# Performance work log

Measured on AMD Instinct MI355X. Metric: run time of the kernel, lower is better.

## Reference

```python
import jax, jax.numpy as jnp
import numpy as np

B = 64           # number of graphs
MAXN = 128       # max nodes per graph (== to_dense_batch n)
D = 512          # hidden_dim
H = 16           # n_attn_heads
HS = D // H      # head_size
SCALE = HS ** -0.5
EPS = 1e-5

# deterministic ragged node counts in [64,128], max exactly 128
_COUNTS = 64 + (np.arange(B) * 37) % 65
NTOT = int(_COUNTS.sum())  # 6148


def setup_inputs() -> dict:
    key = jax.random.key(0)
    ks = jax.random.split(key, 10)
    r = D ** -0.5  # uniform init radius used by the module

    def lin(k):
        kw, kb = jax.random.split(k)
        W = jax.random.uniform(kw, (D, D), minval=-r, maxval=r, dtype=jnp.float32)
        b = jax.random.uniform(kb, (D,), minval=-r, maxval=r, dtype=jnp.float32)
        return W, b

    Wq, bq = lin(ks[0])
    Wk, bk = lin(ks[1])
    Wv, bv = lin(ks[2])
    Wp, bp = lin(ks[3])
    x = jax.random.normal(ks[4], (NTOT, D), dtype=jnp.float32)
    attn_bias = 0.1 * jax.random.normal(ks[5], (B, H, MAXN, MAXN), dtype=jnp.float32)
    batch = jnp.asarray(np.repeat(np.arange(B), _COUNTS), dtype=jnp.int32)
    return {
        "x": x, "attn_bias": attn_bias,
        "Wq": Wq, "bq": bq, "Wk": Wk, "bk": bk, "Wv": Wv, "bv": bv,
        "Wp": Wp, "bp": bp,
        "ln_w": jnp.ones((D,), jnp.float32), "ln_b": jnp.zeros((D,), jnp.float32),
        "batch": batch,
    }


def reference(x, attn_bias, Wq, bq, Wk, bk, Wv, bv, Wp, bp, ln_w, ln_b, batch):
    # eval-mode BiasedSelfAttentionLayer (all dropouts are identity)
    Bn, Hh, n, _ = attn_bias.shape
    N = x.shape[0]
    # to_dense_batch: per-node position inside its graph
    counts = jax.ops.segment_sum(jnp.ones(N, jnp.int32), batch, num_segments=Bn)
    starts = jnp.cumsum(counts) - counts
    pos = jnp.arange(N) - starts[batch]
    x_dense = jnp.zeros((Bn, n, D), x.dtype).at[batch, pos].set(x)  # [B,n,D]
    mask = jnp.zeros((Bn, n), bool).at[batch, pos].set(True)        # [B,n]

    def heads(W, b):
        return (x_dense @ W.T + b).reshape(Bn, n, Hh, HS).transpose(0, 2, 1, 3)

    q = heads(Wq, bq)  # [B,H,n,hs]
    k = heads(Wk, bk)
    v = heads(Wv, bv)

    attn = jnp.einsum("bhqd,bhkd->bhqk", q, k) * SCALE + attn_bias  # [B,H,n,n]
    mask2 = mask[:, None, :, None]  # valid queries
    mask3 = mask[:, None, None, :]  # valid keys
    attn = jnp.where(mask3, attn, -jnp.inf)   # masked_fill(~mask3, -inf)
    attn = jnp.where(mask2, attn, 0.0)        # masked_fill(~mask2, 0.0)
    attn = jax.nn.softmax(attn, axis=-1)
    attn = jnp.where(mask2, attn, 0.0)        # re-zero invalid query rows

    out = jnp.einsum("bhqk,bhkd->bhqd", attn, v)           # [B,H,n,hs]
    out = out.transpose(0, 2, 1, 3).reshape(Bn, n, D)      # [B,n,D]
    out = out @ Wp.T + bp
    out = out[batch, pos] + x                               # scatter back + residual
    # LayerNorm
    mu = out.mean(-1, keepdims=True)
    var = out.var(-1, keepdims=True)
    return (out - mu) / jnp.sqrt(var + EPS) * ln_w + ln_b
```

## Files before the change

### kernel.cpp

```cpp
#include <hip/hip_runtime.h>
#include <math.h>

#define NTOT 6148
#define NB 64
#define DM 512
#define SCALE_F 0.17677669529663687f

typedef __attribute__((ext_vector_type(8))) short bf16x8;
typedef __attribute__((ext_vector_type(4))) float f32x4;

__device__ __forceinline__ short f2bf(float f) {
  union { float f; unsigned u; } v; v.f = f;
  unsigned r = (v.u + 0x7fffu + ((v.u >> 16) & 1u)) >> 16;
  return (short)r;
}

__device__ __forceinline__ void gl_lds16(const void* g, void* l) {
  auto gp = (const __attribute__((address_space(1))) unsigned*)(unsigned long long)(uintptr_t)g;
  auto lp = (__attribute__((address_space(3))) unsigned*)(unsigned long long)(uintptr_t)l;
  __builtin_amdgcn_global_load_lds(gp, lp, 16, 0, 0);
}

__global__ __launch_bounds__(256) void k_cvt(const float* __restrict__ x,
                                             const float* __restrict__ wq,
                                             const float* __restrict__ wk,
                                             const float* __restrict__ wv,
                                             const float* __restrict__ wp,
                                             short* __restrict__ xb,
                                             short* __restrict__ wqb,
                                             short* __restrict__ wkb,
                                             short* __restrict__ wvb,
                                             short* __restrict__ wpb,
                                             const int* __restrict__ batch,
                                             int* __restrict__ starts) {
  const int bid = blockIdx.x;
  if (bid < 25) {
    const int i = bid * 256 + threadIdx.x;
    if (i < NTOT) {
      const int bb = batch[i];
      if (i == 0) starts[bb] = 0;
      else if (batch[i - 1] != bb) starts[bb] = i;
      if (i == NTOT - 1) starts[NB] = NTOT;
    }
  }
  const float* s; short* d; long off;
  if (bid < 1537) {
    s = x; d = xb;
    off = ((long)bid * 256 + threadIdx.x) * 8;
  } else {
    int wi = (bid - 1537) >> 7;
    s = (wi == 0) ? wq : (wi == 1) ? wk : (wi == 2) ? wv : wp;
    d = (wi == 0) ? wqb : (wi == 1) ? wkb : (wi == 2) ? wvb : wpb;
    off = ((long)((bid - 1537) & 127) * 256 + threadIdx.x) * 8;
  }
  float4 v0 = *(const float4*)(s + off);
  float4 v1 = *(const float4*)(s + off + 4);
  bf16x8 o;
  o[0] = f2bf(v0.x); o[1] = f2bf(v0.y); o[2] = f2bf(v0.z); o[3] = f2bf(v0.w);
  o[4] = f2bf(v1.x); o[5] = f2bf(v1.y); o[6] = f2bf(v1.z); o[7] = f2bf(v1.w);
  *(bf16x8*)(d + off) = o;
}

template <int NT, bool BF16OUT>
__global__ __launch_bounds__(256) void k_gemm_mfma(
    const short* __restrict__ Abf,
    const short* __restrict__ W0, const short* __restrict__ W1, const short* __restrict__ W2,
    const float* __restrict__ b0, const float* __restrict__ b1, const float* __restrict__ b2,
    const float* __restrict__ resid, void* __restrict__ Cv, int ldc, int M) {
  constexpr int NF = NT / 32;
  __shared__ __align__(16) short As[2][64][32];
  __shared__ __align__(16) short Bs[2][NT][32];
  const int tid = threadIdx.x;
  const int w = tid >> 6, l = tid & 63;
  const int m0 = blockIdx.y * 64;
  const int n0 = blockIdx.x * NT;
  const int sel = n0 >> 9;
  const short* Wt = (sel == 0) ? W0 : (sel == 1) ? W1 : W2;
  const float* bt = (sel == 0) ? b0 : (sel == 1) ? b1 : b2;
  const int nl0 = n0 & 511;
  const int wr = w >> 1, wc = w & 1;
  const int lr = l >> 2;
  const int lc = (l & 3) * 8;
  const int fr = l & 15, fs = (l >> 4) * 8;

  const long gaA = (long)min(m0 + w * 16 + lr, M - 1) * 512 + lc;
  const long gaB0 = (long)(nl0 + ((NT == 128) ? w * 32 : w * 16) + lr) * 512 + lc;
  const long gaB1 = (long)(nl0 + w * 32 + 16 + lr) * 512 + lc;

  f32x4 acc[2][NF];
#pragma unroll
  for (int m = 0; m < 2; m++)
#pragma unroll
    for (int n = 0; n < NF; n++) acc[m][n] = (f32x4){0.f, 0.f, 0.f, 0.f};

  auto stage = [&](int kt, int buf) {
    const int k0 = kt * 32;
    gl_lds16(Abf + gaA + k0, &As[buf][w * 16][0]);
    if (NT == 128) {
      gl_lds16(Wt + gaB0 + k0, &Bs[buf][w * 32][0]);
      gl_lds16(Wt + gaB1 + k0, &Bs[buf][w * 32 + 16][0]);
    } else {
      gl_lds16(Wt + gaB0 + k0, &Bs[buf][w * 16][0]);
    }
  };
  auto compute = [&](int buf) {
    bf16x8 af[2], bfr[NF];
#pragma unroll
    for (int m = 0; m < 2; m++) af[m] = *(const bf16x8*)&As[buf][wr * 32 + m * 16 + fr][fs];
#pragma unroll
    for (int n = 0; n < NF; n++)
      bfr[n] = *(const bf16x8*)&Bs[buf][wc * (NT / 2) + n * 16 + fr][fs];
#pragma unroll
    for (int m = 0; m < 2; m++)
#pragma unroll
      for (int n = 0; n < NF; n++)
        acc[m][n] = __builtin_amdgcn_mfma_f32_16x16x32_bf16(af[m], bfr[n], acc[m][n], 0, 0, 0);
  };

  stage(0, 0);
  __syncthreads();
  for (int step = 0; step < 16; step++) {
    if (step < 15) stage(step + 1, (step + 1) & 1);
    compute(step & 1);
    __syncthreads();
  }

  const int er = (l >> 4) * 4, ec = l & 15;
#pragma unroll
  for (int n = 0; n < NF; n++) {
    const int col = n0 + wc * (NT / 2) + n * 16 + ec;
    const float bv = bt[col & 511];
#pragma unroll
    for (int m = 0; m < 2; m++) {
      const int rowb = m0 + wr * 32 + m * 16 + er;
#pragma unroll
      for (int j = 0; j < 4; j++) {
        const int row = rowb + j;
        if (row < M) {
          float v = acc[m][n][j] + bv;
          if (resid) v += resid[(long)row * 512 + col];
          if (BF16OUT) ((short*)Cv)[(long)row * ldc + col] = f2bf(v);
          else ((float*)Cv)[(long)row * ldc + col] = v;
        }
      }
    }
  }
}

__global__ __launch_bounds__(256, 2) void k_attn(const short* __restrict__ QKVbf,
                                                 const float* __restrict__ bias,
                                                 const int* __restrict__ starts,
                                                 short* __restrict__ Obf) {
  __shared__ __align__(16) short Ps[4][16][136];
  __shared__ __align__(16) short Vtb[32][136];
  const int id = blockIdx.x;
  const int wg = (id & 7) * 256 + (id >> 3);
  const int b = wg >> 5, qc = (wg >> 4) & 1, h = wg & 15;
  const int tid = threadIdx.x, l = tid & 63, w = tid >> 6;
  const int wq0 = qc * 64 + w * 16;
  const int lg = l >> 4, lk = l & 15, fs = lg * 8;

  const int s0 = starts[b], cnt = starts[b + 1] - s0;
  const bool active = wq0 < cnt;

  const int u = l >> 2, c = (l & 3) * 8;
  const int vr0 = w * 32 + u, vr1 = vr0 + 16;
  const short* vbase = QKVbf + 1024 + h * 32 + c;
  const bf16x8 v0 = *(const bf16x8*)(vbase + (long)(s0 + min(vr0, cnt - 1)) * 1536);
  const bf16x8 v1 = *(const bf16x8*)(vbase + (long)(s0 + min(vr1, cnt - 1)) * 1536);

  bf16x8 aq, bk[8];
  float bv[8][4];
  if (active) {
    const short* qbase = QKVbf + h * 32 + fs;
    aq = *(const bf16x8*)(qbase + (long)(s0 + min(wq0 + lk, cnt - 1)) * 1536);
#pragma unroll
    for (int n = 0; n < 8; n++)
      bk[n] = *(const bf16x8*)(qbase + 512 + (long)(s0 + min(n * 16 + lk, cnt - 1)) * 1536);
    const float* bb = bias + ((long)(b * 16 + h) << 14) + (long)(wq0 + lg * 4) * 128 + lk;
#pragma unroll
    for (int n = 0; n < 8; n++)
#pragma unroll
      for (int j = 0; j < 4; j++) bv[n][j] = bb[j * 128 + n * 16];
  }

#pragma unroll
  for (int i = 0; i < 8; i++) Vtb[c + i][vr0] = v0[i];
#pragma unroll
  for (int i = 0; i < 8; i++) Vtb[c + i][vr1] = v1[i];

  float invs[4];
  if (active) {
    f32x4 S[8];
#pragma unroll
    for (int n = 0; n < 8; n++)
      S[n] = __builtin_amdgcn_mfma_f32_16x16x32_bf16(aq, bk[n],
                                                     (f32x4){0.f, 0.f, 0.f, 0.f}, 0, 0, 0);
#pragma unroll
    for (int n = 0; n < 8; n++) {
      const int k = n * 16 + lk;
      const bool kok = k < cnt;
#pragma unroll
      for (int j = 0; j < 4; j++) {
        const float sv = S[n][j] * SCALE_F + bv[n][j];
        S[n][j] = kok ? sv : -1e30f;
      }
    }
#pragma unroll
    for (int j = 0; j < 4; j++) {
      float mx = S[0][j];
#pragma unroll
      for (int n = 1; n < 8; n++) mx = fmaxf(mx, S[n][j]);
      mx = fmaxf(mx, __shfl_xor(mx, 1));
      mx = fmaxf(mx, __shfl_xor(mx, 2));
      mx = fmaxf(mx, __shfl_xor(mx, 4));
      mx = fmaxf(mx, __shfl_xor(mx, 8));
      float sum = 0.f;
#pragma unroll
      for (int n = 0; n < 8; n++) {
        const float p = __expf(S[n][j] - mx);
        S[n][j] = p;
        sum += p;
      }
      sum += __shfl_xor(sum, 1);
      sum += __shfl_xor(sum, 2);
      sum += __shfl_xor(sum, 4);
      sum += __shfl_xor(sum, 8);
      invs[j] = 1.f / sum;
      const int r = lg * 4 + j;
#pragma unroll
      for (int n = 0; n < 8; n++) Ps[w][r][n * 16 + lk] = f2bf(S[n][j]);
    }
  }

  __syncthreads();
  if (!active) return;

  f32x4 O[2];
#pragma unroll
  for (int dt = 0; dt < 2; dt++) O[dt] = (f32x4){0.f, 0.f, 0.f, 0.f};
#pragma unroll
  for (int kc = 0; kc < 4; kc++) {
    const bf16x8 pa = *(const bf16x8*)&Ps[w][lk][kc * 32 + fs];
#pragma unroll
    for (int dt = 0; dt < 2; dt++) {
      const bf16x8 vb = *(const bf16x8*)&Vtb[dt * 16 + lk][kc * 32 + fs];
      O[dt] = __builtin_amdgcn_mfma_f32_16x16x32_bf16(pa, vb, O[dt], 0, 0, 0);
    }
  }
#pragma unroll
  for (int j = 0; j < 4; j++) {
    const int q = wq0 + lg * 4 + j;
    if (q < cnt) {
      short* orow = Obf + (long)(s0 + q) * 512 + h * 32;
#pragma unroll
      for (int dt = 0; dt < 2; dt++)
        orow[dt * 16 + lk] = f2bf(O[dt][j] * invs[j]);
    }
  }
}

__global__ __launch_bounds__(256) void k_lnp(const float* __restrict__ pre,
                                             const float* __restrict__ lw,
                                             const float* __restrict__ lb,
                                             float* __restrict__ out) {
  const int row = blockIdx.x * 4 + (threadIdx.x >> 6);
  if (row >= NTOT) return;
  const int lane = threadIdx.x & 63;
  const float* pr = pre + (long)row * 512 + lane * 8;
  float4 p0 = *(const float4*)pr;
  float4 p1 = *(const float4*)(pr + 4);
  float v[8] = {p0.x, p0.y, p0.z, p0.w, p1.x, p1.y, p1.z, p1.w};
  float s = 0.f, s2 = 0.f;
#pragma unroll
  for (int j = 0; j < 8; j++) { s += v[j]; s2 += v[j] * v[j]; }
#pragma unroll
  for (int off = 32; off > 0; off >>= 1) {
    s += __shfl_xor(s, off);
    s2 += __shfl_xor(s2, off);
  }
  const float mu = s * (1.f / 512.f);
  const float var = s2 * (1.f / 512.f) - mu * mu;
  const float inv = rsqrtf(var + 1e-5f);
  float4 w0 = *(const float4*)&lw[lane * 8];
  float4 w1 = *(const float4*)&lw[lane * 8 + 4];
  float4 b0 = *(const float4*)&lb[lane * 8];
  float4 b1 = *(const float4*)&lb[lane * 8 + 4];
  float4 o0 = make_float4((v[0] - mu) * inv * w0.x + b0.x, (v[1] - mu) * inv * w0.y + b0.y,
                          (v[2] - mu) * inv * w0.z + b0.z, (v[3] - mu) * inv * w0.w + b0.w);
  float4 o1 = make_float4((v[4] - mu) * inv * w1.x + b1.x, (v[5] - mu) * inv * w1.y + b1.y,
                          (v[6] - mu) * inv * w1.z + b1.z, (v[7] - mu) * inv * w1.w + b1.w);
  float* dst = out + (long)row * 512 + lane * 8;
  *(float4*)dst = o0;
  *(float4*)(dst + 4) = o1;
}

extern "C" void kernel_launch(void* const* d_in, const int* in_sizes, int n_in,
                              void* d_out, int out_size, void* d_ws, size_t ws_size,
                              hipStream_t stream) {
  const float* x = (const float*)d_in[0];
  const float* attn_bias = (const float*)d_in[1];
  const float* Wq = (const float*)d_in[2];
  const float* bq = (const float*)d_in[3];
  const float* Wk = (const float*)d_in[4];
  const float* bk = (const float*)d_in[5];
  const float* Wv = (const float*)d_in[6];
  const float* bv = (const float*)d_in[7];
  const float* Wp = (const float*)d_in[8];
  const float* bp = (const float*)d_in[9];
  const float* ln_w = (const float*)d_in[10];
  const float* ln_b = (const float*)d_in[11];
  const int* batch = (const int*)d_in[12];
  float* out = (float*)d_out;

  char* ws = (char*)d_ws;
  int* starts = (int*)ws;
  short* Xbf = (short*)(ws + 512);
  short* Wqb = Xbf + (long)NTOT * 512;
  short* Wkb = Wqb + 512 * 512;
  short* Wvb = Wkb + 512 * 512;
  short* Wpb = Wvb + 512 * 512;
  short* QKVbf = Wpb + 512 * 512;
  short* Obf = Xbf;
  float* proj = (float*)QKVbf;

  k_cvt<<<1537 + 4 * 128, 256, 0, stream>>>(x, Wq, Wk, Wv, Wp, Xbf, Wqb, Wkb, Wvb, Wpb,
                                            batch, starts);

  dim3 gq(12, (NTOT + 63) / 64);
  k_gemm_mfma<128, true><<<gq, 256, 0, stream>>>(Xbf, Wqb, Wkb, Wvb, bq, bk, bv,
                                                 nullptr, QKVbf, 1536, NTOT);

  k_attn<<<2048, 256, 0, stream>>>(QKVbf, attn_bias, starts, Obf);

  dim3 gp(8, (NTOT + 63) / 64);
  k_gemm_mfma<64, false><<<gp, 256, 0, stream>>>(Obf, Wpb, Wpb, Wpb, bp, bp, bp,
                                                 x, proj, 512, NTOT);

  k_lnp<<<(NTOT + 3) / 4, 256, 0, stream>>>(proj, ln_w, ln_b, out);
}
```

Baseline: 75.60 us.

## Transpose score MFMA for vectorized bias loads and store bf16 projection output

The QK^T MFMA operands are swapped so each lane holds four consecutive keys for one query row. This lets the attention bias be read as float4, the softmax reductions need only two cross-lane shuffles, and probabilities can be normalized before being written to LDS as bf16x4. Separately, the output projection GEMM now writes bf16 instead of fp32, which halves the traffic into the LayerNorm kernel. That bf16 intermediate, which includes the residual, reduces precision before LayerNorm. It is also unclear whether the bf16 GEMM template path adds x as a residual the same way the fp32 path did.

```diff
diff --git a/kernel.cpp b/kernel.cpp
--- a/kernel.cpp
+++ b/kernel.cpp
@@ -7,12 +7,18 @@
 #define SCALE_F 0.17677669529663687f
 
 typedef __attribute__((ext_vector_type(8))) short bf16x8;
+typedef __attribute__((ext_vector_type(4))) short bf16x4;
 typedef __attribute__((ext_vector_type(4))) float f32x4;
 
 __device__ __forceinline__ short f2bf(float f) {
   union { float f; unsigned u; } v; v.f = f;
   unsigned r = (v.u + 0x7fffu + ((v.u >> 16) & 1u)) >> 16;
   return (short)r;
+}
+__device__ __forceinline__ float bf2f(short s) {
+  union { unsigned u; float f; } v;
+  v.u = ((unsigned)(unsigned short)s) << 16;
+  return v.f;
 }
 
 __device__ __forceinline__ void gl_lds16(const void* g, void* l) {
@@ -170,18 +176,16 @@
   const bf16x8 v1 = *(const bf16x8*)(vbase + (long)(s0 + min(vr1, cnt - 1)) * 1536);
 
   bf16x8 aq, bk[8];
-  float bv[8][4];
+  float4 bv4[8];
   if (active) {
     const short* qbase = QKVbf + h * 32 + fs;
     aq = *(const bf16x8*)(qbase + (long)(s0 + min(wq0 + lk, cnt - 1)) * 1536);
 #pragma unroll
     for (int n = 0; n < 8; n++)
       bk[n] = *(const bf16x8*)(qbase + 512 + (long)(s0 + min(n * 16 + lk, cnt - 1)) * 1536);
-    const float* bb = bias + ((long)(b * 16 + h) << 14) + (long)(wq0 + lg * 4) * 128 + lk;
-#pragma unroll
-    for (int n = 0; n < 8; n++)
-#pragma unroll
-      for (int j = 0; j < 4; j++) bv[n][j] = bb[j * 128 + n * 16];
+    const float* bb = bias + ((long)(b * 16 + h) << 14) + (long)(wq0 + lk) * 128 + lg * 4;
+#pragma unroll
+    for (int n = 0; n < 8; n++) bv4[n] = *(const float4*)(bb + n * 16);
   }
 
 #pragma unroll
@@ -189,47 +193,49 @@
 #pragma unroll
   for (int i = 0; i < 8; i++) Vtb[c + i][vr1] = v1[i];
 
-  float invs[4];
   if (active) {
     f32x4 S[8];
 #pragma unroll
     for (int n = 0; n < 8; n++)
-      S[n] = __builtin_amdgcn_mfma_f32_16x16x32_bf16(aq, bk[n],
+      S[n] = __builtin_amdgcn_mfma_f32_16x16x32_bf16(bk[n], aq,
                                                      (f32x4){0.f, 0.f, 0.f, 0.f}, 0, 0, 0);
 #pragma unroll
     for (int n = 0; n < 8; n++) {
-      const int k = n * 16 + lk;
-      const bool kok = k < cnt;
-#pragma unroll
-      for (int j = 0; j < 4; j++) {
-        const float sv = S[n][j] * SCALE_F + bv[n][j];
-        S[n][j] = kok ? sv : -1e30f;
-      }
-    }
-#pragma unroll
-    for (int j = 0; j < 4; j++) {
-      float mx = S[0][j];
-#pragma unroll
-      for (int n = 1; n < 8; n++) mx = fmaxf(mx, S[n][j]);
-      mx = fmaxf(mx, __shfl_xor(mx, 1));
-      mx = fmaxf(mx, __shfl_xor(mx, 2));
-      mx = fmaxf(mx, __shfl_xor(mx, 4));
-      mx = fmaxf(mx, __shfl_xor(mx, 8));
-      float sum = 0.f;
-#pragma unroll
-      for (int n = 0; n < 8; n++) {
-        const float p = __expf(S[n][j] - mx);
-        S[n][j] = p;
-        sum += p;
-      }
-      sum += __shfl_xor(sum, 1);
-      sum += __shfl_xor(sum, 2);
-      sum += __shfl_xor(sum, 4);
-      sum += __shfl_xor(sum, 8);
-      invs[j] = 1.f / sum;
-      const int r = lg * 4 + j;
-#pragma unroll
-      for (int n = 0; n < 8; n++) Ps[w][r][n * 16 + lk] = f2bf(S[n][j]);
+      const int kb = n * 16 + lg * 4;
+      S[n][0] = (kb + 0 < cnt) ? S[n][0] * SCALE_F + bv4[n].x : -1e30f;
+      S[n][1] = (kb + 1 < cnt) ? S[n][1] * SCALE_F + bv4[n].y : -1e30f;
+      S[n][2] = (kb + 2 < cnt) ? S[n][2] * SCALE_F + bv4[n].z : -1e30f;
+      S[n][3] = (kb + 3 < cnt) ? S[n][3] * SCALE_F + bv4[n].w : -1e30f;
+    }
+    float pm[8];
+#pragma unroll
+    for (int n = 0; n < 8; n++)
+      pm[n] = fmaxf(fmaxf(S[n][0], S[n][1]), fmaxf(S[n][2], S[n][3]));
+    float mx = fmaxf(fmaxf(fmaxf(pm[0], pm[1]), fmaxf(pm[2], pm[3])),
+                     fmaxf(fmaxf(pm[4], pm[5]), fmaxf(pm[6], pm[7])));
+    mx = fmaxf(mx, __shfl_xor(mx, 16));
+    mx = fmaxf(mx, __shfl_xor(mx, 32));
+    float ps[8];
+#pragma unroll
+    for (int n = 0; n < 8; n++) {
+      S[n][0] = __expf(S[n][0] - mx);
+      S[n][1] = __expf(S[n][1] - mx);
+      S[n][2] = __expf(S[n][2] - mx);
+      S[n][3] = __expf(S[n][3] - mx);
+      ps[n] = (S[n][0] + S[n][1]) + (S[n][2] + S[n][3]);
+    }
+    float sum = ((ps[0] + ps[1]) + (ps[2] + ps[3])) + ((ps[4] + ps[5]) + (ps[6] + ps[7]));
+    sum += __shfl_xor(sum, 16);
+    sum += __shfl_xor(sum, 32);
+    const float inv = 1.f / sum;
+#pragma unroll
+    for (int n = 0; n < 8; n++) {
+      bf16x4 p4;
+      p4[0] = f2bf(S[n][0] * inv);
+      p4[1] = f2bf(S[n][1] * inv);
+      p4[2] = f2bf(S[n][2] * inv);
+      p4[3] = f2bf(S[n][3] * inv);
+      *(bf16x4*)&Ps[w][lk][n * 16 + lg * 4] = p4;
     }
   }
 
@@ -255,22 +261,22 @@
       short* orow = Obf + (long)(s0 + q) * 512 + h * 32;
 #pragma unroll
       for (int dt = 0; dt < 2; dt++)
-        orow[dt * 16 + lk] = f2bf(O[dt][j] * invs[j]);
-    }
-  }
-}
-
-__global__ __launch_bounds__(256) void k_lnp(const float* __restrict__ pre,
+        orow[dt * 16 + lk] = f2bf(O[dt][j]);
+    }
+  }
+}
+
+__global__ __launch_bounds__(256) void k_lnp(const short* __restrict__ pre,
                                              const float* __restrict__ lw,
                                              const float* __restrict__ lb,
                                              float* __restrict__ out) {
   const int row = blockIdx.x * 4 + (threadIdx.x >> 6);
   if (row >= NTOT) return;
   const int lane = threadIdx.x & 63;
-  const float* pr = pre + (long)row * 512 + lane * 8;
-  float4 p0 = *(const float4*)pr;
-  float4 p1 = *(const float4*)(pr + 4);
-  float v[8] = {p0.x, p0.y, p0.z, p0.w, p1.x, p1.y, p1.z, p1.w};
+  const bf16x8 pv = *(const bf16x8*)(pre + (long)row * 512 + lane * 8);
+  float v[8];
+#pragma unroll
+  for (int j = 0; j < 8; j++) v[j] = bf2f(pv[j]);
   float s = 0.f, s2 = 0.f;
 #pragma unroll
   for (int j = 0; j < 8; j++) { s += v[j]; s2 += v[j] * v[j]; }
@@ -322,7 +328,7 @@
   short* Wpb = Wvb + 512 * 512;
   short* QKVbf = Wpb + 512 * 512;
   short* Obf = Xbf;
-  float* proj = (float*)QKVbf;
+  short* projbf = QKVbf;
 
   k_cvt<<<1537 + 4 * 128, 256, 0, stream>>>(x, Wq, Wk, Wv, Wp, Xbf, Wqb, Wkb, Wvb, Wpb,
                                             batch, starts);
@@ -334,8 +340,8 @@
   k_attn<<<2048, 256, 0, stream>>>(QKVbf, attn_bias, starts, Obf);
 
   dim3 gp(8, (NTOT + 63) / 64);
-  k_gemm_mfma<64, false><<<gp, 256, 0, stream>>>(Obf, Wpb, Wpb, Wpb, bp, bp, bp,
-                                                 x, proj, 512, NTOT);
-
-  k_lnp<<<(NTOT + 3) / 4, 256, 0, stream>>>(proj, ln_w, ln_b, out);
-}
+  k_gemm_mfma<64, true><<<gp, 256, 0, stream>>>(Obf, Wpb, Wpb, Wpb, bp, bp, bp,
+                                                x, projbf, 512, NTOT);
+
+  k_lnp<<<(NTOT + 3) / 4, 256, 0, stream>>>(projbf, ln_w, ln_b, out);
+}
```

New measurement: 76.88 us. No clear change (+1.7%).
